# Performance work log

Hardware: AMD Instinct MI355X
Metric: run time of the kernel (lower is better)

The kernel has to match this reference:

```python
import jax, jax.numpy as jnp
import numpy as np

B, N, E, D, NUM_RBF, CUTOFF = 2, 25000, 400000, 128, 64, 15.0


def setup_inputs() -> dict:
    key = jax.random.key(0)
    ks = jax.random.split(key, 8)
    atom_features = jax.random.normal(ks[0], (B, N, D), dtype=jnp.float32)
    distances = jax.random.uniform(ks[1], (B, E), dtype=jnp.float32) * CUTOFF
    idx_j = jax.random.randint(ks[2], (E,), 0, N)
    seg_i = jnp.sort(jax.random.randint(ks[3], (E,), 0, N))
    # RBF params (as in RBFExpansion.__init__)
    centers = jnp.asarray(np.linspace(0.0, CUTOFF, NUM_RBF), dtype=jnp.float32)
    gamma = jnp.full((NUM_RBF,), 10.0, dtype=jnp.float32)
    # filter-MLP params (Dense default glorot_uniform init; random normal scaled is fine for reference)
    W1 = jax.random.normal(ks[4], (NUM_RBF, D), dtype=jnp.float32) / np.sqrt(NUM_RBF)
    b1 = jnp.zeros((D,), dtype=jnp.float32)
    W2 = jax.random.normal(ks[5], (D, D), dtype=jnp.float32) / np.sqrt(D)
    b2 = jnp.zeros((D,), dtype=jnp.float32)
    return {"atom_features": atom_features, "distances": distances,
            "idx_j": idx_j, "seg_i": seg_i,
            "centers": centers, "gamma": gamma,
            "W1": W1, "b1": b1, "W2": W2, "b2": b2}


def _ssp(x):
    # shifted softplus: softplus(x) - log(2)
    return jax.nn.softplus(x) - jnp.log(2.0).astype(x.dtype)


def reference(atom_features, distances, idx_j, seg_i, centers, gamma, W1, b1, W2, b2):
    n_atoms = atom_features.shape[1]
    # RBF expansion: [B, E, NUM_RBF]
    d = distances[..., None]
    rbf = jnp.exp(-gamma * (d - centers) ** 2)
    # filter-generating MLP: [B, E, D]
    filters = _ssp(rbf @ W1 + b1)
    filters = _ssp(filters @ W2 + b2)
    # gather neighbor features along atom axis: [B, E, D]
    neigh = jnp.take(atom_features, idx_j, axis=1)
    msgs = neigh * filters
    # segment-sum over edges into destination atoms: [B, N, D]
    agg = jax.ops.segment_sum(jnp.swapaxes(msgs, 0, 1), seg_i, num_segments=n_atoms)
    return jnp.swapaxes(agg, 0, 1)
```

## Files before the change

kernel.cpp:

```cpp
#include <hip/hip_runtime.h>
#include <math.h>

#define B_ 2
#define N_ 25000
#define E_ 400000
#define D_ 128
#define NRBF 64

#define TPB 256
#define TILE 64
#define NTILES 25
#define EPB (TILE * NTILES)
#define WCH (EPB / 4)
#define GCH (EPB / 16)
#define NBLK (E_ / EPB)

typedef short bf8   __attribute__((ext_vector_type(8)));
typedef float f32x4 __attribute__((ext_vector_type(4)));
typedef float vf8   __attribute__((ext_vector_type(8)));
typedef float vf16  __attribute__((ext_vector_type(16)));

__device__ __forceinline__ short f2bf(float f) {
    union { float f; unsigned u; } v; v.f = f;
    unsigned r = (v.u + 0x7FFFu + ((v.u >> 16) & 1u)) >> 16;
    return (short)r;
}
__device__ __forceinline__ float ssp(float x) {
    return fmaxf(x, 0.0f) + __logf(1.0f + __expf(-fabsf(x))) - 0.69314718056f;
}

__global__ __launch_bounds__(TPB, 2)
void cfconv_kernel(const float* __restrict__ af,
                   const float* __restrict__ dist,
                   const int*   __restrict__ idx_j,
                   const int*   __restrict__ seg_i,
                   const float* __restrict__ centers,
                   const float* __restrict__ gam,
                   const float* __restrict__ W1,
                   const float* __restrict__ b1,
                   const float* __restrict__ W2,
                   const float* __restrict__ b2,
                   float* __restrict__ out)
{
    const int t    = threadIdx.x;
    const int lane = t & 63;
    const int w    = t >> 6;
    const int g    = lane >> 4;
    const int c0   = lane & 15;
    const int b    = blockIdx.y;
    const int e0   = blockIdx.x * EPB;

    __shared__ __align__(16) short W1f[2 * 4 * D_ * 8];
    __shared__ __align__(16) short W2f[4 * 4 * D_ * 8];
    __shared__ __align__(16) short A1 [4 * 2 * 4 * 16 * 8];
    __shared__ __align__(16) short A2 [4 * 4 * 4 * 16 * 8];
    __shared__ float gs[NRBF], cs[NRBF];

    for (int i = t; i < NRBF * D_; i += TPB) {
        const int k = i >> 7, n = i & 127;
        W1f[(((k >> 5) * 4 + ((k >> 3) & 3)) * D_ + n) * 8 + (k & 7)] = f2bf(W1[i]);
    }
    for (int i = t; i < D_ * D_; i += TPB) {
        const int k = i >> 7, n = i & 127;
        W2f[(((k >> 5) * 4 + ((k >> 3) & 3)) * D_ + n) * 8 + (k & 7)] = f2bf(W2[i]);
    }
    if (t < NRBF) { gs[t] = gam[t]; cs[t] = centers[t]; }
    __syncthreads();

    vf8 b1r, b2r;
    #pragma unroll
    for (int nt = 0; nt < 8; ++nt) {
        b1r[nt] = b1[nt * 16 + c0];
        b2r[nt] = b2[nt * 16 + c0];
    }
    const int el = t >> 2, kq = t & 3;
    const int we = el >> 4, me = el & 15;
    vf16 gkr, ckr;
    #pragma unroll
    for (int kk = 0; kk < 16; ++kk) { gkr[kk] = gs[kq * 16 + kk]; ckr[kk] = cs[kq * 16 + kk]; }

    const float* dist_b = dist + (size_t)b * E_;
    const float* af_b   = af   + (size_t)b * N_ * D_;
    float*       out_b  = out  + (size_t)b * N_ * D_;

    const int ebase = e0 + w * WCH + g * GCH;

    int cur_seg = -1;
    vf8 pend = (vf8)0.0f;

    for (int s = 0; s < NTILES; ++s) {
        {
            const int e = e0 + we * WCH + (me >> 2) * GCH + s * 4 + (me & 3);
            const float dd = dist_b[e];
            short rb[16];
            #pragma unroll
            for (int kk = 0; kk < 16; ++kk) {
                const float x = dd - ckr[kk];
                rb[kk] = f2bf(__expf(-gkr[kk] * x * x));
            }
            bf8 lo, hi;
            #pragma unroll
            for (int j = 0; j < 8; ++j) { lo[j] = rb[j]; hi[j] = rb[8 + j]; }
            const int base = (((we * 2 + (kq >> 1)) * 4 + (kq & 1) * 2) * 16 + me) * 8;
            *(bf8*)&A1[base]            = lo;
            *(bf8*)&A1[base + 16 * 8]   = hi;
        }
        __syncthreads();

        {
            const bf8 a0 = *(const bf8*)&A1[(((w * 2 + 0) * 4 + g) * 16 + c0) * 8];
            const bf8 a1 = *(const bf8*)&A1[(((w * 2 + 1) * 4 + g) * 16 + c0) * 8];
            f32x4 hh[8];
            #pragma unroll
            for (int nt = 0; nt < 8; ++nt) {
                const bf8 w0 = *(const bf8*)&W1f[((0 * 4 + g) * D_ + nt * 16 + c0) * 8];
                const bf8 w1 = *(const bf8*)&W1f[((1 * 4 + g) * D_ + nt * 16 + c0) * 8];
                f32x4 acc = {0.f, 0.f, 0.f, 0.f};
                acc = __builtin_amdgcn_mfma_f32_16x16x32_bf16(a0, w0, acc, 0, 0, 0);
                acc = __builtin_amdgcn_mfma_f32_16x16x32_bf16(a1, w1, acc, 0, 0, 0);
                hh[nt] = acc;
            }
            #pragma unroll
            for (int nt = 0; nt < 8; ++nt) {
                const int shb = (((w * 4 + (nt >> 1)) * 4 + ((nt & 1) * 2 + (c0 >> 3))) * 16) * 8 + (c0 & 7);
                #pragma unroll
                for (int r = 0; r < 4; ++r) {
                    const float hv = ssp(hh[nt][r] + b1r[nt]);
                    A2[shb + (g * 4 + r) * 8] = f2bf(hv);
                }
            }
        }
        __syncthreads();

        {
            const bf8 p0 = *(const bf8*)&A2[(((w * 4 + 0) * 4 + g) * 16 + c0) * 8];
            const bf8 p1 = *(const bf8*)&A2[(((w * 4 + 1) * 4 + g) * 16 + c0) * 8];
            const bf8 p2 = *(const bf8*)&A2[(((w * 4 + 2) * 4 + g) * 16 + c0) * 8];
            const bf8 p3 = *(const bf8*)&A2[(((w * 4 + 3) * 4 + g) * 16 + c0) * 8];
            f32x4 facc[8];
            #pragma unroll
            for (int nt = 0; nt < 8; ++nt) {
                const bf8 w0 = *(const bf8*)&W2f[((0 * 4 + g) * D_ + nt * 16 + c0) * 8];
                const bf8 w1 = *(const bf8*)&W2f[((1 * 4 + g) * D_ + nt * 16 + c0) * 8];
                const bf8 w2 = *(const bf8*)&W2f[((2 * 4 + g) * D_ + nt * 16 + c0) * 8];
                const bf8 w3 = *(const bf8*)&W2f[((3 * 4 + g) * D_ + nt * 16 + c0) * 8];
                f32x4 acc = {0.f, 0.f, 0.f, 0.f};
                acc = __builtin_amdgcn_mfma_f32_16x16x32_bf16(p0, w0, acc, 0, 0, 0);
                acc = __builtin_amdgcn_mfma_f32_16x16x32_bf16(p1, w1, acc, 0, 0, 0);
                acc = __builtin_amdgcn_mfma_f32_16x16x32_bf16(p2, w2, acc, 0, 0, 0);
                acc = __builtin_amdgcn_mfma_f32_16x16x32_bf16(p3, w3, acc, 0, 0, 0);
                facc[nt] = acc;
            }
            #pragma unroll
            for (int r = 0; r < 4; ++r) {
                const int e  = ebase + s * 4 + r;
                const int j  = idx_j[e];
                const int sg = seg_i[e];
                const float* row = af_b + (size_t)j * D_ + c0;
                vf8 msg;
                #pragma unroll
                for (int nt = 0; nt < 8; ++nt) {
                    const float fv = ssp(facc[nt][r] + b2r[nt]);
                    msg[nt] = row[nt * 16] * fv;
                }
                if (sg != cur_seg) {
                    if (cur_seg >= 0) {
                        float* o = out_b + (size_t)cur_seg * D_ + c0;
                        #pragma unroll
                        for (int nt = 0; nt < 8; ++nt) atomicAdd(o + nt * 16, pend[nt]);
                    }
                    cur_seg = sg;
                    pend = msg;
                } else {
                    pend += msg;
                }
            }
        }
    }
    if (cur_seg >= 0) {
        float* o = out_b + (size_t)cur_seg * D_ + c0;
        #pragma unroll
        for (int nt = 0; nt < 8; ++nt) atomicAdd(o + nt * 16, pend[nt]);
    }
}

extern "C" void kernel_launch(void* const* d_in, const int* in_sizes, int n_in,
                              void* d_out, int out_size, void* d_ws, size_t ws_size,
                              hipStream_t stream) {
    const float* af      = (const float*)d_in[0];
    const float* dist    = (const float*)d_in[1];
    const int*   idx_j   = (const int*)d_in[2];
    const int*   seg_i   = (const int*)d_in[3];
    const float* centers = (const float*)d_in[4];
    const float* gam     = (const float*)d_in[5];
    const float* W1      = (const float*)d_in[6];
    const float* b1      = (const float*)d_in[7];
    const float* W2      = (const float*)d_in[8];
    const float* b2      = (const float*)d_in[9];
    float* out = (float*)d_out;

    hipMemsetAsync(out, 0, (size_t)out_size * sizeof(float), stream);

    dim3 grid(NBLK, B_);
    cfconv_kernel<<<grid, TPB, 0, stream>>>(af, dist, idx_j, seg_i,
                                            centers, gam, W1, b1, W2, b2, out);
}
```

Before: 281.9 us.

## Compute RBF MFMA operands in registers and drop block barriers

Each lane now builds its RBF A-operand fragment directly in registers (exp2 with pre-scaled gamma, truncating bf16 pack), so the A1 shared buffer and its barrier go away. W1 is held in registers as MFMA B fragments with a permuted output-column mapping. The intermediate activations go to a per-wave, XOR-swizzled A2 region, so the remaining block-wide syncs are removed and only wave-local LDS traffic is left. In exchange the kernel uses more registers, which may hurt occupancy, and the RBF and hidden activations are rounded with truncation-style bf16 packing.

Result: slower. 483.3 us (+71.4%).

```diff
diff --git a/kernel.cpp b/kernel.cpp
--- a/kernel.cpp
+++ b/kernel.cpp
@@ -8,25 +8,36 @@
 #define NRBF 64
 
 #define TPB 256
-#define TILE 64
 #define NTILES 25
-#define EPB (TILE * NTILES)
-#define WCH (EPB / 4)
-#define GCH (EPB / 16)
+#define WCH 400
+#define GCH 100
+#define EPB (4 * WCH)
 #define NBLK (E_ / EPB)
 
-typedef short bf8   __attribute__((ext_vector_type(8)));
-typedef float f32x4 __attribute__((ext_vector_type(4)));
-typedef float vf8   __attribute__((ext_vector_type(8)));
-typedef float vf16  __attribute__((ext_vector_type(16)));
-
+typedef short bf8    __attribute__((ext_vector_type(8)));
+typedef float f32x4  __attribute__((ext_vector_type(4)));
+typedef float vf8    __attribute__((ext_vector_type(8)));
+typedef unsigned int u32;
+typedef u32 u32x4    __attribute__((ext_vector_type(4)));
+
+__device__ __forceinline__ u32 pack2(float hi, float lo) {
+    union { float f; u32 u; } a, b; a.f = hi; b.f = lo;
+    return __builtin_amdgcn_perm(a.u + 0x8000u, b.u + 0x8000u, 0x07060302u);
+}
+__device__ __forceinline__ u32 pack2rne(float hi, float lo) {
+    union { float f; u32 u; } a, b; a.f = hi; b.f = lo;
+    u32 au = a.u + 0x7FFFu + ((a.u >> 16) & 1u);
+    u32 bu = b.u + 0x7FFFu + ((b.u >> 16) & 1u);
+    return __builtin_amdgcn_perm(au, bu, 0x07060302u);
+}
 __device__ __forceinline__ short f2bf(float f) {
-    union { float f; unsigned u; } v; v.f = f;
-    unsigned r = (v.u + 0x7FFFu + ((v.u >> 16) & 1u)) >> 16;
-    return (short)r;
+    union { float f; u32 u; } v; v.f = f;
+    return (short)((v.u + 0x7FFFu + ((v.u >> 16) & 1u)) >> 16);
 }
 __device__ __forceinline__ float ssp(float x) {
-    return fmaxf(x, 0.0f) + __logf(1.0f + __expf(-fabsf(x))) - 0.69314718056f;
+    float t = __expf(-fabsf(x));
+    float l = __logf(1.0f + t);
+    return (fmaxf(x, 0.0f) - 0.69314718056f) + l;
 }
 
 __global__ __launch_bounds__(TPB, 2)
@@ -50,130 +61,135 @@
     const int b    = blockIdx.y;
     const int e0   = blockIdx.x * EPB;
 
-    __shared__ __align__(16) short W1f[2 * 4 * D_ * 8];
     __shared__ __align__(16) short W2f[4 * 4 * D_ * 8];
-    __shared__ __align__(16) short A1 [4 * 2 * 4 * 16 * 8];
-    __shared__ __align__(16) short A2 [4 * 4 * 4 * 16 * 8];
-    __shared__ float gs[NRBF], cs[NRBF];
-
-    for (int i = t; i < NRBF * D_; i += TPB) {
-        const int k = i >> 7, n = i & 127;
-        W1f[(((k >> 5) * 4 + ((k >> 3) & 3)) * D_ + n) * 8 + (k & 7)] = f2bf(W1[i]);
-    }
+    __shared__ __align__(16) short A2[4][16][16][8];
+
     for (int i = t; i < D_ * D_; i += TPB) {
         const int k = i >> 7, n = i & 127;
         W2f[(((k >> 5) * 4 + ((k >> 3) & 3)) * D_ + n) * 8 + (k & 7)] = f2bf(W2[i]);
     }
-    if (t < NRBF) { gs[t] = gam[t]; cs[t] = centers[t]; }
     __syncthreads();
 
-    vf8 b1r, b2r;
+    bf8 w1r[16];
     #pragma unroll
-    for (int nt = 0; nt < 8; ++nt) {
-        b1r[nt] = b1[nt * 16 + c0];
-        b2r[nt] = b2[nt * 16 + c0];
-    }
-    const int el = t >> 2, kq = t & 3;
-    const int we = el >> 4, me = el & 15;
-    vf16 gkr, ckr;
+    for (int cc = 0; cc < 2; ++cc) {
+        vf8 row[8];
+        #pragma unroll
+        for (int j = 0; j < 8; ++j)
+            row[j] = *(const vf8*)&W1[(size_t)(cc * 32 + g * 8 + j) * D_ + 8 * c0];
+        #pragma unroll
+        for (int nt = 0; nt < 8; ++nt) {
+            u32x4 q;
+            #pragma unroll
+            for (int p = 0; p < 4; ++p)
+                q[p] = pack2rne(row[2 * p + 1][nt], row[2 * p][nt]);
+            w1r[cc * 8 + nt] = __builtin_bit_cast(bf8, q);
+        }
+    }
+
+    const vf8 b1r = *(const vf8*)&b1[8 * c0];
+    vf8 b2r;
     #pragma unroll
-    for (int kk = 0; kk < 16; ++kk) { gkr[kk] = gs[kq * 16 + kk]; ckr[kk] = cs[kq * 16 + kk]; }
+    for (int nt = 0; nt < 8; ++nt) b2r[nt] = b2[nt * 16 + c0];
+
+    vf8 gla, glb, cla, clb;
+    #pragma unroll
+    for (int j = 0; j < 8; ++j) {
+        gla[j] = gam[g * 8 + j]      * 1.44269504f;
+        glb[j] = gam[32 + g * 8 + j] * 1.44269504f;
+        cla[j] = centers[g * 8 + j];
+        clb[j] = centers[32 + g * 8 + j];
+    }
 
     const float* dist_b = dist + (size_t)b * E_;
     const float* af_b   = af   + (size_t)b * N_ * D_;
     float*       out_b  = out  + (size_t)b * N_ * D_;
 
+    const int eArow = e0 + w * WCH + (c0 >> 2) * GCH + (c0 & 3);
     const int ebase = e0 + w * WCH + g * GCH;
 
     int cur_seg = -1;
     vf8 pend = (vf8)0.0f;
 
     for (int s = 0; s < NTILES; ++s) {
+        const float dd = dist_b[eArow + s * 4];
+        u32x4 qa, qb;
+        #pragma unroll
+        for (int p = 0; p < 4; ++p) {
+            float x0 = dd - cla[2 * p];     float v0 = exp2f(-gla[2 * p]     * x0 * x0);
+            float x1 = dd - cla[2 * p + 1]; float v1 = exp2f(-gla[2 * p + 1] * x1 * x1);
+            qa[p] = pack2(v1, v0);
+            float y0 = dd - clb[2 * p];     float u0 = exp2f(-glb[2 * p]     * y0 * y0);
+            float y1 = dd - clb[2 * p + 1]; float u1 = exp2f(-glb[2 * p + 1] * y1 * y1);
+            qb[p] = pack2(u1, u0);
+        }
+        const bf8 a0 = __builtin_bit_cast(bf8, qa);
+        const bf8 a1 = __builtin_bit_cast(bf8, qb);
+
+        f32x4 hh[8];
+        #pragma unroll
+        for (int nt = 0; nt < 8; ++nt) {
+            f32x4 acc = {0.f, 0.f, 0.f, 0.f};
+            acc = __builtin_amdgcn_mfma_f32_16x16x32_bf16(a0, w1r[nt],     acc, 0, 0, 0);
+            acc = __builtin_amdgcn_mfma_f32_16x16x32_bf16(a1, w1r[8 + nt], acc, 0, 0, 0);
+            hh[nt] = acc;
+        }
+
+        #pragma unroll
+        for (int r = 0; r < 4; ++r) {
+            u32x4 q;
+            #pragma unroll
+            for (int p = 0; p < 4; ++p) {
+                float v0 = ssp(hh[2 * p][r]     + b1r[2 * p]);
+                float v1 = ssp(hh[2 * p + 1][r] + b1r[2 * p + 1]);
+                q[p] = pack2(v1, v0);
+            }
+            const int mphys = (g * 4 + r) ^ (c0 & 7);
+            *(bf8*)&A2[w][c0][mphys][0] = __builtin_bit_cast(bf8, q);
+        }
+
+        f32x4 facc[8];
         {
-            const int e = e0 + we * WCH + (me >> 2) * GCH + s * 4 + (me & 3);
-            const float dd = dist_b[e];
-            short rb[16];
-            #pragma unroll
-            for (int kk = 0; kk < 16; ++kk) {
-                const float x = dd - ckr[kk];
-                rb[kk] = f2bf(__expf(-gkr[kk] * x * x));
-            }
-            bf8 lo, hi;
-            #pragma unroll
-            for (int j = 0; j < 8; ++j) { lo[j] = rb[j]; hi[j] = rb[8 + j]; }
-            const int base = (((we * 2 + (kq >> 1)) * 4 + (kq & 1) * 2) * 16 + me) * 8;
-            *(bf8*)&A1[base]            = lo;
-            *(bf8*)&A1[base + 16 * 8]   = hi;
-        }
-        __syncthreads();
-
-        {
-            const bf8 a0 = *(const bf8*)&A1[(((w * 2 + 0) * 4 + g) * 16 + c0) * 8];
-            const bf8 a1 = *(const bf8*)&A1[(((w * 2 + 1) * 4 + g) * 16 + c0) * 8];
-            f32x4 hh[8];
+            bf8 pfr[4];
+            #pragma unroll
+            for (int cc = 0; cc < 4; ++cc) {
+                const int c0w = cc * 4 + g;
+                pfr[cc] = *(const bf8*)&A2[w][c0w][c0 ^ (c0w & 7)][0];
+            }
             #pragma unroll
             for (int nt = 0; nt < 8; ++nt) {
-                const bf8 w0 = *(const bf8*)&W1f[((0 * 4 + g) * D_ + nt * 16 + c0) * 8];
-                const bf8 w1 = *(const bf8*)&W1f[((1 * 4 + g) * D_ + nt * 16 + c0) * 8];
                 f32x4 acc = {0.f, 0.f, 0.f, 0.f};
-                acc = __builtin_amdgcn_mfma_f32_16x16x32_bf16(a0, w0, acc, 0, 0, 0);
-                acc = __builtin_amdgcn_mfma_f32_16x16x32_bf16(a1, w1, acc, 0, 0, 0);
-                hh[nt] = acc;
-            }
+                #pragma unroll
+                for (int cc = 0; cc < 4; ++cc) {
+                    const bf8 wf = *(const bf8*)&W2f[((cc * 4 + g) * D_ + nt * 16 + c0) * 8];
+                    acc = __builtin_amdgcn_mfma_f32_16x16x32_bf16(pfr[cc], wf, acc, 0, 0, 0);
+                }
+                facc[nt] = acc;
+            }
+        }
+
+        #pragma unroll
+        for (int r = 0; r < 4; ++r) {
+            const int e  = ebase + s * 4 + r;
+            const int j  = idx_j[e];
+            const int sg = seg_i[e];
+            const float* row = af_b + (size_t)j * D_ + c0;
+            vf8 msg;
             #pragma unroll
             for (int nt = 0; nt < 8; ++nt) {
-                const int shb = (((w * 4 + (nt >> 1)) * 4 + ((nt & 1) * 2 + (c0 >> 3))) * 16) * 8 + (c0 & 7);
-                #pragma unroll
-                for (int r = 0; r < 4; ++r) {
-                    const float hv = ssp(hh[nt][r] + b1r[nt]);
-                    A2[shb + (g * 4 + r) * 8] = f2bf(hv);
+                const float fv = ssp(facc[nt][r] + b2r[nt]);
+                msg[nt] = row[nt * 16] * fv;
+            }
+            if (sg != cur_seg) {
+                if (cur_seg >= 0) {
+                    float* o = out_b + (size_t)cur_seg * D_ + c0;
+                    #pragma unroll
+                    for (int nt = 0; nt < 8; ++nt) atomicAdd(o + nt * 16, pend[nt]);
                 }
-            }
-        }
-        __syncthreads();
-
-        {
-            const bf8 p0 = *(const bf8*)&A2[(((w * 4 + 0) * 4 + g) * 16 + c0) * 8];
-            const bf8 p1 = *(const bf8*)&A2[(((w * 4 + 1) * 4 + g) * 16 + c0) * 8];
-            const bf8 p2 = *(const bf8*)&A2[(((w * 4 + 2) * 4 + g) * 16 + c0) * 8];
-            const bf8 p3 = *(const bf8*)&A2[(((w * 4 + 3) * 4 + g) * 16 + c0) * 8];
-            f32x4 facc[8];
-            #pragma unroll
-            for (int nt = 0; nt < 8; ++nt) {
-                const bf8 w0 = *(const bf8*)&W2f[((0 * 4 + g) * D_ + nt * 16 + c0) * 8];
-                const bf8 w1 = *(const bf8*)&W2f[((1 * 4 + g) * D_ + nt * 16 + c0) * 8];
-                const bf8 w2 = *(const bf8*)&W2f[((2 * 4 + g) * D_ + nt * 16 + c0) * 8];
-                const bf8 w3 = *(const bf8*)&W2f[((3 * 4 + g) * D_ + nt * 16 + c0) * 8];
-                f32x4 acc = {0.f, 0.f, 0.f, 0.f};
-                acc = __builtin_amdgcn_mfma_f32_16x16x32_bf16(p0, w0, acc, 0, 0, 0);
-                acc = __builtin_amdgcn_mfma_f32_16x16x32_bf16(p1, w1, acc, 0, 0, 0);
-                acc = __builtin_amdgcn_mfma_f32_16x16x32_bf16(p2, w2, acc, 0, 0, 0);
-                acc = __builtin_amdgcn_mfma_f32_16x16x32_bf16(p3, w3, acc, 0, 0, 0);
-                facc[nt] = acc;
-            }
-            #pragma unroll
-            for (int r = 0; r < 4; ++r) {
-                const int e  = ebase + s * 4 + r;
-                const int j  = idx_j[e];
-                const int sg = seg_i[e];
-                const float* row = af_b + (size_t)j * D_ + c0;
-                vf8 msg;
-                #pragma unroll
-                for (int nt = 0; nt < 8; ++nt) {
-                    const float fv = ssp(facc[nt][r] + b2r[nt]);
-                    msg[nt] = row[nt * 16] * fv;
-                }
-                if (sg != cur_seg) {
-                    if (cur_seg >= 0) {
-                        float* o = out_b + (size_t)cur_seg * D_ + c0;
-                        #pragma unroll
-                        for (int nt = 0; nt < 8; ++nt) atomicAdd(o + nt * 16, pend[nt]);
-                    }
-                    cur_seg = sg;
-                    pend = msg;
-                } else {
-                    pend += msg;
-                }
+                cur_seg = sg;
+                pend = msg;
+            } else {
+                pend += msg;
             }
         }
     }
```
